# Optimization experiments

Hardware: AMD Instinct MI355X
Metric: run time of the kernel (lower is better)

Reference implementation:

```python
import jax, jax.numpy as jnp
import numpy as np

N = 100000      # nodes
E = 400000      # edges
DIN, DH, DOUT = 32, 128, 1
EPS = 1e-5


def _lin_init(key, fan_in, shape):
    s = 1.0 / np.sqrt(fan_in)
    return jax.random.uniform(key, shape, jnp.float32, -s, s)


def setup_inputs() -> dict:
    key = jax.random.key(0)
    ks = jax.random.split(key, 24)
    x = jax.random.normal(ks[0], (N, DIN), jnp.float32)
    edge_index = jax.random.randint(ks[1], (2, E), 0, N, dtype=jnp.int64)
    d = {"x": x, "edge_index": edge_index}
    dims = [(DIN, DH), (DH, DH), (DH, DOUT)]
    for i, (din, dout) in enumerate(dims, start=1):
        d[f"W{i}"] = _lin_init(ks[2 * i], din, (din, dout))
        d[f"b{i}"] = _lin_init(ks[2 * i + 1], din, (dout,))
        d[f"g{i}"] = jnp.ones((dout,), jnp.float32)    # BatchNorm weight
        d[f"bt{i}"] = jnp.zeros((dout,), jnp.float32)  # BatchNorm bias
        d[f"lw{i}"] = jnp.ones((dout,), jnp.float32)   # LayerNorm weight
        d[f"lb{i}"] = jnp.zeros((dout,), jnp.float32)  # LayerNorm bias
    return d


def reference(x, edge_index, W1, b1, g1, bt1, lw1, lb1,
              W2, b2, g2, bt2, lw2, lb2,
              W3, b3, g3, bt3, lw3, lb3):
    n = x.shape[0]
    loop = jnp.arange(n, dtype=edge_index.dtype)
    src = jnp.concatenate([edge_index[0], loop])  # self-loops added (GCNConv default)
    dst = jnp.concatenate([edge_index[1], loop])
    deg = jax.ops.segment_sum(jnp.ones(src.shape[0], x.dtype), dst, num_segments=n)
    dinv = jnp.where(deg > 0, jax.lax.rsqrt(deg), 0.0)
    norm = dinv[src] * dinv[dst]  # D^{-1/2} (A+I) D^{-1/2} edge weights

    def gcn(h, W, b):
        h = h @ W
        agg = jax.ops.segment_sum(h[src] * norm[:, None], dst, num_segments=n)
        return agg + b

    def bn(h, g, b):  # BatchNorm1d, training-mode batch stats (biased var)
        m = h.mean(0)
        v = h.var(0)
        return (h - m) * jax.lax.rsqrt(v + EPS) * g + b

    def inorm(h):  # PyG InstanceNorm, single graph, affine=False
        m = h.mean(0)
        v = h.var(0)
        return (h - m) * jax.lax.rsqrt(v + EPS)

    def lnorm(h, w, b):  # PyG LayerNorm, mode='graph': stats over all nodes+channels
        m = h.mean()
        v = h.var()
        return (h - m) * jax.lax.rsqrt(v + EPS) * w + b

    h = jax.nn.relu(lnorm(inorm(bn(gcn(x, W1, b1), g1, bt1)), lw1, lb1))
    h = jax.nn.relu(lnorm(inorm(bn(gcn(h, W2, b2), g2, bt2)), lw2, lb2))
    h = lnorm(inorm(bn(gcn(h, W3, b3), g3, bt3)), lw3, lb3)
    return h.flatten()
```

## Files before the change

kernel.cpp:

```cpp
#include <hip/hip_runtime.h>
#include <cstddef>

#define EPS 1e-5f

typedef __attribute__((ext_vector_type(8))) short bf16x8;
typedef __attribute__((ext_vector_type(8))) unsigned short u16x8;
typedef __attribute__((ext_vector_type(4))) float f32x4;

__device__ inline short f2bf(float f) {
    union { float f; unsigned u; } v;
    v.f = f;
    unsigned r = v.u + 0x7fff + ((v.u >> 16) & 1);
    return (short)(r >> 16);
}
__device__ inline float bf2f(unsigned short s) {
    union { unsigned u; float f; } v;
    v.u = ((unsigned)s) << 16;
    return v.f;
}

__global__ void prep_kernel(const float* __restrict__ W1, const float* __restrict__ W2,
                            unsigned short* __restrict__ Wt1, unsigned short* __restrict__ Wt2,
                            int* __restrict__ counts, float* __restrict__ sums,
                            unsigned long long* __restrict__ state, int* __restrict__ ticket,
                            int n) {
    int o = blockIdx.x * blockDim.x + threadIdx.x;
    if (o < n) counts[o] = 0;
    if (o < 516) sums[o] = 0.f;
    if (o < 128) state[o] = 0ULL;
    if (o == 0) *ticket = 0;
    if (o < 32 * 128) {
        int c = o / 32, k = o % 32;
        Wt1[o] = (unsigned short)f2bf(W1[(size_t)k * 128 + c]);
    } else if (o < 32 * 128 + 128 * 128) {
        int o2 = o - 32 * 128;
        int c = o2 / 128, k = o2 % 128;
        Wt2[o2] = (unsigned short)f2bf(W2[(size_t)k * 128 + c]);
    }
}

__global__ void hist_kernel(const int* __restrict__ dst, int E, int* __restrict__ counts) {
    int i = blockIdx.x * blockDim.x + threadIdx.x;
    if (i < E) atomicAdd(&counts[dst[i]], 1);
}

__global__ __launch_bounds__(1024) void scan_lookback(const int* __restrict__ counts,
                                                      int* __restrict__ rowptr,
                                                      int* __restrict__ cur,
                                                      float* __restrict__ dinv,
                                                      unsigned long long* __restrict__ state,
                                                      int* __restrict__ ticket, int n, int E) {
    __shared__ int sh[1024];
    __shared__ int sbid, sexcl;
    int t = threadIdx.x;
    if (t == 0) sbid = atomicAdd(ticket, 1);
    __syncthreads();
    int bid = sbid;
    int g = bid * 1024 + t;
    int v = (g < n) ? counts[g] : 0;
    sh[t] = v;
    __syncthreads();
    for (int off = 1; off < 1024; off <<= 1) {
        int add = (t >= off) ? sh[t - off] : 0;
        __syncthreads();
        sh[t] += add;
        __syncthreads();
    }
    int total = sh[1023];
    if (t == 0) {
        if (bid == 0) {
            atomicExch(&state[0], (2ULL << 32) | (unsigned)total);
            sexcl = 0;
        } else {
            atomicExch(&state[bid], (1ULL << 32) | (unsigned)total);
            int excl = 0;
            int j = bid - 1;
            while (true) {
                unsigned long long s;
                do { s = atomicAdd(&state[j], 0ULL); } while ((s >> 32) == 0);
                excl += (int)(s & 0xffffffffULL);
                if ((s >> 32) == 2ULL) break;
                j--;
            }
            atomicExch(&state[bid], (2ULL << 32) | (unsigned)(excl + total));
            sexcl = excl;
        }
    }
    __syncthreads();
    int excl = sexcl;
    if (g < n) {
        int r = excl + sh[t] - v;
        rowptr[g] = r;
        cur[g] = r;
        dinv[g] = rsqrtf((float)counts[g] + 1.0f);
    }
    if (g == 0) rowptr[n] = E;
}

__global__ void fill_kernel(const int* __restrict__ src, const int* __restrict__ dst, int E,
                            int* __restrict__ cur, const float* __restrict__ dinv,
                            int* __restrict__ esrc, float* __restrict__ ewt) {
    int e = blockIdx.x * blockDim.x + threadIdx.x;
    if (e < E) {
        int d = dst[e];
        int s = src[e];
        int p = atomicAdd(&cur[d], 1);
        esrc[p] = s;
        ewt[p] = dinv[s] * dinv[d];
    }
}

template <int K, bool NORM, bool STATS>
__global__ __launch_bounds__(256) void gemm_mfma(const unsigned short* __restrict__ hb,
                                                 const unsigned short* __restrict__ Wt,
                                                 const float* __restrict__ ss,
                                                 unsigned short* __restrict__ outb,
                                                 float* __restrict__ sums, int n) {
    int wid = (blockIdx.x * 256 + threadIdx.x) >> 6;
    int wv = (threadIdx.x >> 6);
    int lane = threadIdx.x & 63;
    int m = lane & 15;
    int qd = lane >> 4;
    int r0 = wid * 32;
    if (!STATS && r0 >= n) return;

    f32x4 acc[2][8];
#pragma unroll
    for (int rt = 0; rt < 2; rt++)
#pragma unroll
        for (int ct = 0; ct < 8; ct++) acc[rt][ct] = (f32x4){0.f, 0.f, 0.f, 0.f};

    if (r0 < n) {
#pragma unroll
        for (int q = 0; q < K / 32; q++) {
            int k0 = q * 32 + qd * 8;
            bf16x8 a[2];
#pragma unroll
            for (int rt = 0; rt < 2; rt++) {
                int r = r0 + rt * 16 + m;
                bf16x8 av = (bf16x8){0, 0, 0, 0, 0, 0, 0, 0};
                if (r < n) av = *(const bf16x8*)(hb + (size_t)r * K + k0);
                if (NORM) {
#pragma unroll
                    for (int j = 0; j < 8; j++) {
                        float f = bf2f((unsigned short)av[j]);
                        f = fmaxf(fmaf(f, ss[k0 + j], ss[K + k0 + j]), 0.f);
                        av[j] = f2bf(f);
                    }
                }
                a[rt] = av;
            }
#pragma unroll
            for (int ct = 0; ct < 8; ct++) {
                bf16x8 b = *(const bf16x8*)(Wt + (size_t)(ct * 16 + m) * K + k0);
                acc[0][ct] = __builtin_amdgcn_mfma_f32_16x16x32_bf16(a[0], b, acc[0][ct], 0, 0, 0);
                acc[1][ct] = __builtin_amdgcn_mfma_f32_16x16x32_bf16(a[1], b, acc[1][ct], 0, 0, 0);
            }
        }
#pragma unroll
        for (int rt = 0; rt < 2; rt++)
#pragma unroll
            for (int i = 0; i < 4; i++) {
                int r = r0 + rt * 16 + qd * 4 + i;
                if (r < n) {
#pragma unroll
                    for (int ct = 0; ct < 8; ct++)
                        outb[(size_t)r * 128 + ct * 16 + m] = (unsigned short)f2bf(acc[rt][ct][i]);
                }
            }
    }

    if (STATS) {
        __shared__ float ls[4][128], lq[4][128];
#pragma unroll
        for (int ct = 0; ct < 8; ct++) {
            float s = 0.f, q = 0.f;
#pragma unroll
            for (int rt = 0; rt < 2; rt++)
#pragma unroll
                for (int i = 0; i < 4; i++) {
                    float v = acc[rt][ct][i];
                    s += v;
                    q += v * v;
                }
            s += __shfl_xor(s, 16, 64);
            s += __shfl_xor(s, 32, 64);
            q += __shfl_xor(q, 16, 64);
            q += __shfl_xor(q, 32, 64);
            if (qd == 0) {
                ls[wv][ct * 16 + m] = s;
                lq[wv][ct * 16 + m] = q;
            }
        }
        __syncthreads();
        int t = threadIdx.x;
        if (t < 128) {
            atomicAdd(&sums[t], ls[0][t] + ls[1][t] + ls[2][t] + ls[3][t]);
        } else {
            int c = t - 128;
            atomicAdd(&sums[128 + c], lq[0][c] + lq[1][c] + lq[2][c] + lq[3][c]);
        }
    }
}

__global__ void gemv_norm_bf(const unsigned short* __restrict__ hb, const float* __restrict__ W,
                             const float* __restrict__ ss, float* __restrict__ out, int n) {
    int gid = blockIdx.x * blockDim.x + threadIdx.x;
    int wid = gid >> 6, lane = gid & 63;
    int nw = (gridDim.x * blockDim.x) >> 6;
    int c = lane * 2;
    float w0 = W[c], w1 = W[c + 1];
    float s0 = ss[c], s1 = ss[c + 1];
    float t0 = ss[128 + c], t1 = ss[128 + c + 1];
    for (int r = wid; r < n; r += nw) {
        ushort2 u = ((const ushort2*)(hb + (size_t)r * 128))[lane];
        float a = fmaxf(fmaf(bf2f(u.x), s0, t0), 0.f);
        float b = fmaxf(fmaf(bf2f(u.y), s1, t1), 0.f);
        float v = fmaf(a, w0, b * w1);
#pragma unroll
        for (int off = 32; off > 0; off >>= 1) v += __shfl_down(v, off, 64);
        if (lane == 0) out[r] = v;
    }
}

__global__ __launch_bounds__(256) void agg128_bf(const unsigned short* __restrict__ tmp,
                                                 const int* __restrict__ rowptr,
                                                 const int* __restrict__ esrc,
                                                 const float* __restrict__ ewt,
                                                 const float* __restrict__ dinv,
                                                 unsigned short* __restrict__ agg, int n) {
    int node = (blockIdx.x << 4) + (threadIdx.x >> 4);
    if (node >= n) return;
    int co = (threadIdx.x & 15) << 3;
    float di = dinv[node];
    float d2 = di * di;
    u16x8 t = *(const u16x8*)(tmp + ((size_t)node << 7) + co);
    float acc[8];
#pragma unroll
    for (int k = 0; k < 8; k++) acc[k] = bf2f(t[k]) * d2;
    int j = rowptr[node], je = rowptr[node + 1];
    for (; j + 8 <= je; j += 8) {
        int s[8];
        float w[8];
        u16x8 v[8];
#pragma unroll
        for (int k = 0; k < 8; k++) { s[k] = esrc[j + k]; w[k] = ewt[j + k]; }
#pragma unroll
        for (int k = 0; k < 8; k++) v[k] = *(const u16x8*)(tmp + ((size_t)s[k] << 7) + co);
#pragma unroll
        for (int k = 0; k < 8; k++)
#pragma unroll
            for (int c = 0; c < 8; c++) acc[c] = fmaf(bf2f(v[k][c]), w[k], acc[c]);
    }
    if (j + 4 <= je) {
        int s[4];
        float w[4];
        u16x8 v[4];
#pragma unroll
        for (int k = 0; k < 4; k++) { s[k] = esrc[j + k]; w[k] = ewt[j + k]; }
#pragma unroll
        for (int k = 0; k < 4; k++) v[k] = *(const u16x8*)(tmp + ((size_t)s[k] << 7) + co);
#pragma unroll
        for (int k = 0; k < 4; k++)
#pragma unroll
            for (int c = 0; c < 8; c++) acc[c] = fmaf(bf2f(v[k][c]), w[k], acc[c]);
        j += 4;
    }
    for (; j < je; j++) {
        int s = esrc[j];
        float w = ewt[j];
        u16x8 v = *(const u16x8*)(tmp + ((size_t)s << 7) + co);
#pragma unroll
        for (int c = 0; c < 8; c++) acc[c] = fmaf(bf2f(v[c]), w, acc[c]);
    }
    u16x8 o;
#pragma unroll
    for (int k = 0; k < 8; k++) o[k] = (unsigned short)f2bf(acc[k]);
    *(u16x8*)(agg + ((size_t)node << 7) + co) = o;
}

__global__ __launch_bounds__(256) void stats128_bf(const unsigned short* __restrict__ a,
                                                   float* __restrict__ sums, int n) {
    __shared__ float ls[16][128], lq[16][128];
    int t = threadIdx.x;
    int rg = t >> 4;
    int cg = t & 15;
    float s[8], q[8];
#pragma unroll
    for (int k = 0; k < 8; k++) { s[k] = 0.f; q[k] = 0.f; }
    for (int r = blockIdx.x * 16 + rg; r < n; r += gridDim.x * 16) {
        u16x8 v = *(const u16x8*)(a + (size_t)r * 128 + cg * 8);
#pragma unroll
        for (int k = 0; k < 8; k++) {
            float f = bf2f(v[k]);
            s[k] += f;
            q[k] = fmaf(f, f, q[k]);
        }
    }
#pragma unroll
    for (int k = 0; k < 8; k++) {
        ls[rg][cg * 8 + k] = s[k];
        lq[rg][cg * 8 + k] = q[k];
    }
    __syncthreads();
    if (t < 128) {
        float v = 0.f;
#pragma unroll
        for (int i = 0; i < 16; i++) v += ls[i][t];
        atomicAdd(&sums[t], v);
    } else {
        int c = t - 128;
        float v = 0.f;
#pragma unroll
        for (int i = 0; i < 16; i++) v += lq[i][c];
        atomicAdd(&sums[128 + c], v);
    }
}

__global__ __launch_bounds__(256) void agg32_f(const float* __restrict__ x,
                                               const int* __restrict__ rowptr,
                                               const int* __restrict__ esrc,
                                               const float* __restrict__ ewt,
                                               const float* __restrict__ dinv,
                                               unsigned short* __restrict__ xab, int n) {
    int g = threadIdx.x >> 3;
    int lane = threadIdx.x & 7;
    int node = blockIdx.x * 32 + g;
    if (node >= n) return;
    int co = lane << 2;
    float di = dinv[node];
    float d2 = di * di;
    float4 a = *(const float4*)(x + ((size_t)node << 5) + co);
    a.x *= d2; a.y *= d2; a.z *= d2; a.w *= d2;
    int j = rowptr[node], je = rowptr[node + 1];
    for (; j + 4 <= je; j += 4) {
        int s0 = esrc[j], s1 = esrc[j + 1], s2 = esrc[j + 2], s3 = esrc[j + 3];
        float w0 = ewt[j], w1 = ewt[j + 1], w2 = ewt[j + 2], w3 = ewt[j + 3];
        float4 v0 = *(const float4*)(x + ((size_t)s0 << 5) + co);
        float4 v1 = *(const float4*)(x + ((size_t)s1 << 5) + co);
        float4 v2 = *(const float4*)(x + ((size_t)s2 << 5) + co);
        float4 v3 = *(const float4*)(x + ((size_t)s3 << 5) + co);
        a.x = fmaf(v0.x, w0, a.x); a.y = fmaf(v0.y, w0, a.y);
        a.z = fmaf(v0.z, w0, a.z); a.w = fmaf(v0.w, w0, a.w);
        a.x = fmaf(v1.x, w1, a.x); a.y = fmaf(v1.y, w1, a.y);
        a.z = fmaf(v1.z, w1, a.z); a.w = fmaf(v1.w, w1, a.w);
        a.x = fmaf(v2.x, w2, a.x); a.y = fmaf(v2.y, w2, a.y);
        a.z = fmaf(v2.z, w2, a.z); a.w = fmaf(v2.w, w2, a.w);
        a.x = fmaf(v3.x, w3, a.x); a.y = fmaf(v3.y, w3, a.y);
        a.z = fmaf(v3.z, w3, a.z); a.w = fmaf(v3.w, w3, a.w);
    }
    for (; j < je; j++) {
        int s = esrc[j];
        float w = ewt[j];
        float4 v = *(const float4*)(x + ((size_t)s << 5) + co);
        a.x = fmaf(v.x, w, a.x); a.y = fmaf(v.y, w, a.y);
        a.z = fmaf(v.z, w, a.z); a.w = fmaf(v.w, w, a.w);
    }
    ushort4 o;
    o.x = (unsigned short)f2bf(a.x);
    o.y = (unsigned short)f2bf(a.y);
    o.z = (unsigned short)f2bf(a.z);
    o.w = (unsigned short)f2bf(a.w);
    ((ushort4*)(xab + ((size_t)node << 5)))[lane] = o;
}

__global__ void agg1_stats(const float* __restrict__ tmp, const int* __restrict__ rowptr,
                           const int* __restrict__ esrc, const float* __restrict__ ewt,
                           const float* __restrict__ dinv, float* __restrict__ out,
                           float* __restrict__ part, int n) {
    int i = blockIdx.x * blockDim.x + threadIdx.x;
    float acc = 0.f;
    if (i < n) {
        float di = dinv[i];
        acc = tmp[i] * di * di;
        int j = rowptr[i], je = rowptr[i + 1];
        for (; j + 4 <= je; j += 4) {
            int s0 = esrc[j], s1 = esrc[j + 1], s2 = esrc[j + 2], s3 = esrc[j + 3];
            float w0 = ewt[j], w1 = ewt[j + 1], w2 = ewt[j + 2], w3 = ewt[j + 3];
            float v0 = tmp[s0], v1 = tmp[s1], v2 = tmp[s2], v3 = tmp[s3];
            acc = fmaf(v0, w0, acc);
            acc = fmaf(v1, w1, acc);
            acc = fmaf(v2, w2, acc);
            acc = fmaf(v3, w3, acc);
        }
        for (; j < je; j++) acc = fmaf(tmp[esrc[j]], ewt[j], acc);
        out[i] = acc;
    }
    float s = acc, q = acc * acc;
#pragma unroll
    for (int off = 32; off > 0; off >>= 1) {
        s += __shfl_down(s, off, 64);
        q += __shfl_down(q, off, 64);
    }
    if ((threadIdx.x & 63) == 0) {
        int wgid = (blockIdx.x * blockDim.x + threadIdx.x) >> 6;
        part[2 * wgid] = s;
        part[2 * wgid + 1] = q;
    }
}

__global__ __launch_bounds__(256) void reduce_part(const float* __restrict__ part,
                                                   float* __restrict__ sums, int nw) {
    __shared__ float ls[256], lq[256];
    int t = threadIdx.x;
    float s = 0.f, q = 0.f;
    for (int i = t; i < nw; i += 256) {
        s += part[2 * i];
        q += part[2 * i + 1];
    }
    ls[t] = s;
    lq[t] = q;
    __syncthreads();
    for (int off = 128; off > 0; off >>= 1) {
        if (t < off) {
            ls[t] += ls[t + off];
            lq[t] += lq[t + off];
        }
        __syncthreads();
    }
    if (t == 0) {
        sums[0] = ls[0];
        sums[1] = lq[0];
    }
}

__global__ void apply1_kernel(const float* __restrict__ sums, const float* __restrict__ g,
                              const float* __restrict__ lw, const float* __restrict__ lb,
                              const float* __restrict__ a, float* __restrict__ out, int n) {
    int i = blockIdx.x * blockDim.x + threadIdx.x;
    if (i >= n) return;
    float m = sums[0] / n;
    float v = sums[1] / n - m * m;
    v = v < 0.f ? 0.f : v;
    float bs = rsqrtf(v + EPS) * g[0];
    float vz = v * bs * bs;
    float t = bs * rsqrtf(vz + EPS);
    float GV = v * t * t;
    float S = t * rsqrtf(GV + EPS) * lw[0];
    float T = lb[0] - m * S;
    out[i] = fmaf(a[i], S, T);
}

template <int C>
__global__ void finalize_kernel(const float* __restrict__ sums, const float* __restrict__ g,
                                const float* __restrict__ lw, const float* __restrict__ lb,
                                float* __restrict__ ss, int n) {
    __shared__ float vt2[C];
    int c = threadIdx.x;
    float m = sums[c] / n;
    float v = sums[C + c] / n - m * m;
    v = v < 0.f ? 0.f : v;
    float gc = g[c];
    float bs = rsqrtf(v + EPS) * gc;
    float vz = v * bs * bs;
    float t = bs * rsqrtf(vz + EPS);
    vt2[c] = v * t * t;
    __syncthreads();
    if (c == 0) {
        float gv = 0.f;
        for (int i = 0; i < C; i++) gv += vt2[i];
        vt2[0] = gv / C;
    }
    __syncthreads();
    float GV = vt2[0];
    float S = t * rsqrtf(GV + EPS) * lw[c];
    ss[c] = S;
    ss[C + c] = lb[c] - m * S;
}

extern "C" void kernel_launch(void* const* d_in, const int* in_sizes, int n_in,
                              void* d_out, int out_size, void* d_ws, size_t ws_size,
                              hipStream_t stream) {
    const float* x = (const float*)d_in[0];
    const int* ei = (const int*)d_in[1];
    int n = in_sizes[0] / 32;
    int E = in_sizes[1] / 2;
    const int* src = ei;
    const int* dstp = ei + E;
    const float* W1 = (const float*)d_in[2];
    const float* g1 = (const float*)d_in[4];
    const float* lw1 = (const float*)d_in[6];
    const float* lb1 = (const float*)d_in[7];
    const float* W2 = (const float*)d_in[8];
    const float* g2 = (const float*)d_in[10];
    const float* lw2 = (const float*)d_in[12];
    const float* lb2 = (const float*)d_in[13];
    const float* W3 = (const float*)d_in[14];
    const float* g3 = (const float*)d_in[16];
    const float* lw3 = (const float*)d_in[18];
    const float* lb3 = (const float*)d_in[19];
    float* out = (float*)d_out;

    char* p = (char*)d_ws;
    int* counts = (int*)p;             p += (size_t)n * 4;
    int* cur = (int*)p;                p += (size_t)n * 4;
    int* rowptr = (int*)p;             p += (size_t)(n + 4) * 4;
    unsigned long long* state = (unsigned long long*)p;  p += 128 * 8;
    int* ticket = (int*)p;             p += 4 * 4;
    int* esrc = (int*)p;               p += (size_t)E * 4;
    float* ewt = (float*)p;            p += (size_t)E * 4;
    float* dinv = (float*)p;           p += (size_t)n * 4;
    unsigned short* Wt1 = (unsigned short*)p;  p += 128 * 32 * 2;
    unsigned short* Wt2 = (unsigned short*)p;  p += 128 * 128 * 2;
    unsigned short* xa = (unsigned short*)p;   p += (size_t)n * 32 * 2;
    unsigned short* h1 = (unsigned short*)p;   p += (size_t)n * 128 * 2;
    unsigned short* t2 = (unsigned short*)p;   p += (size_t)n * 128 * 2;
    unsigned short* a2 = (unsigned short*)p;   p += (size_t)n * 128 * 2;
    float* t3 = (float*)p;             p += (size_t)n * 4;
    float* a3 = (float*)p;             p += (size_t)n * 4;
    float* sums1 = (float*)p;          p += 256 * 4;
    float* sums2 = (float*)p;          p += 256 * 4;
    float* sums3 = (float*)p;          p += 4 * 4;
    float* ss1 = (float*)p;            p += 256 * 4;
    float* ss2 = (float*)p;            p += 256 * 4;
    float* part3 = (float*)p;          p += ((size_t)(n + 255) / 256) * 4 * 2 * 4;

    int B = (n + 1023) / 1024;

    prep_kernel<<<(n + 255) / 256, 256, 0, stream>>>(W1, W2, Wt1, Wt2, counts, sums1,
                                                     state, ticket, n);
    hist_kernel<<<(E + 255) / 256, 256, 0, stream>>>(dstp, E, counts);
    scan_lookback<<<B, 1024, 0, stream>>>(counts, rowptr, cur, dinv, state, ticket, n, E);
    fill_kernel<<<(E + 255) / 256, 256, 0, stream>>>(src, dstp, E, cur, dinv, esrc, ewt);

    int mblk = ((n + 31) / 32 + 3) / 4;

    agg32_f<<<(n + 31) / 32, 256, 0, stream>>>(x, rowptr, esrc, ewt, dinv, xa, n);
    gemm_mfma<32, false, true><<<mblk, 256, 0, stream>>>(xa, Wt1, nullptr, h1, sums1, n);
    finalize_kernel<128><<<1, 128, 0, stream>>>(sums1, g1, lw1, lb1, ss1, n);

    gemm_mfma<128, true, false><<<mblk, 256, 0, stream>>>(h1, Wt2, ss1, t2, nullptr, n);
    agg128_bf<<<(n + 15) / 16, 256, 0, stream>>>(t2, rowptr, esrc, ewt, dinv, a2, n);
    stats128_bf<<<512, 256, 0, stream>>>(a2, sums2, n);
    finalize_kernel<128><<<1, 128, 0, stream>>>(sums2, g2, lw2, lb2, ss2, n);

    int ablk1 = (n + 255) / 256;
    gemv_norm_bf<<<1024, 256, 0, stream>>>(a2, W3, ss2, t3, n);
    agg1_stats<<<ablk1, 256, 0, stream>>>(t3, rowptr, esrc, ewt, dinv, a3, part3, n);
    reduce_part<<<1, 256, 0, stream>>>(part3, sums3, ablk1 * 4);
    apply1_kernel<<<(n + 255) / 256, 256, 0, stream>>>(sums3, g3, lw3, lb3, a3, out, n);
}
```

Before: 307.7 us.

## Pack edge src/weight into int2 and fuse norm finalize kernels into consumers

Edge source indices and normalized weights are stored together as int2 so the aggregation kernels issue one 8-byte load per edge instead of two separate loads. The standalone finalize and reduce kernels are removed: each consuming block (the second GEMM, the GEMV, and the final apply) recomputes the BN/InstanceNorm/LayerNorm scale/shift from the raw sums in shared memory. This drops several tiny launches and intermediate buffers, at the cost of redundant per-block finalize work and an extra serial reduction plus barriers at block start.

```diff
diff --git a/kernel.cpp b/kernel.cpp
--- a/kernel.cpp
+++ b/kernel.cpp
@@ -26,7 +26,7 @@
                             int n) {
     int o = blockIdx.x * blockDim.x + threadIdx.x;
     if (o < n) counts[o] = 0;
-    if (o < 516) sums[o] = 0.f;
+    if (o < 512) sums[o] = 0.f;
     if (o < 128) state[o] = 0ULL;
     if (o == 0) *ticket = 0;
     if (o < 32 * 128) {
@@ -99,23 +99,60 @@
 
 __global__ void fill_kernel(const int* __restrict__ src, const int* __restrict__ dst, int E,
                             int* __restrict__ cur, const float* __restrict__ dinv,
-                            int* __restrict__ esrc, float* __restrict__ ewt) {
+                            int2* __restrict__ edge) {
     int e = blockIdx.x * blockDim.x + threadIdx.x;
     if (e < E) {
         int d = dst[e];
         int s = src[e];
         int p = atomicAdd(&cur[d], 1);
-        esrc[p] = s;
-        ewt[p] = dinv[s] * dinv[d];
-    }
+        edge[p] = make_int2(s, __float_as_int(dinv[s] * dinv[d]));
+    }
+}
+
+__device__ inline void finalize_ch(float sum, float sumsq, float g, int n,
+                                   float& m, float& t, float& vt2) {
+    m = sum / n;
+    float v = sumsq / n - m * m;
+    v = v < 0.f ? 0.f : v;
+    float bs = rsqrtf(v + EPS) * g;
+    float vz = v * bs * bs;
+    t = bs * rsqrtf(vz + EPS);
+    vt2 = v * t * t;
 }
 
 template <int K, bool NORM, bool STATS>
 __global__ __launch_bounds__(256) void gemm_mfma(const unsigned short* __restrict__ hb,
                                                  const unsigned short* __restrict__ Wt,
-                                                 const float* __restrict__ ss,
+                                                 const float* __restrict__ sums_in,
+                                                 const float* __restrict__ gw,
+                                                 const float* __restrict__ lw,
+                                                 const float* __restrict__ lb,
                                                  unsigned short* __restrict__ outb,
-                                                 float* __restrict__ sums, int n) {
+                                                 float* __restrict__ sums_out, int n) {
+    __shared__ float sh_ss[NORM ? 256 : 1];
+    __shared__ float sh_v[NORM ? 128 : 1];
+    if (NORM) {
+        int t = threadIdx.x;
+        float m, tt, vt2;
+        if (t < 128) {
+            finalize_ch(sums_in[t], sums_in[128 + t], gw[t], n, m, tt, vt2);
+            sh_v[t] = vt2;
+        }
+        __syncthreads();
+        if (t == 0) {
+            float gv = 0.f;
+            for (int i = 0; i < 128; i++) gv += sh_v[i];
+            sh_v[0] = gv / 128.f;
+        }
+        __syncthreads();
+        if (t < 128) {
+            float S = tt * rsqrtf(sh_v[0] + EPS) * lw[t];
+            sh_ss[t] = S;
+            sh_ss[128 + t] = lb[t] - m * S;
+        }
+        __syncthreads();
+    }
+
     int wid = (blockIdx.x * 256 + threadIdx.x) >> 6;
     int wv = (threadIdx.x >> 6);
     int lane = threadIdx.x & 63;
@@ -144,7 +181,7 @@
 #pragma unroll
                     for (int j = 0; j < 8; j++) {
                         float f = bf2f((unsigned short)av[j]);
-                        f = fmaxf(fmaf(f, ss[k0 + j], ss[K + k0 + j]), 0.f);
+                        f = fmaxf(fmaf(f, sh_ss[k0 + j], sh_ss[K + k0 + j]), 0.f);
                         av[j] = f2bf(f);
                     }
                 }
@@ -195,23 +232,51 @@
         __syncthreads();
         int t = threadIdx.x;
         if (t < 128) {
-            atomicAdd(&sums[t], ls[0][t] + ls[1][t] + ls[2][t] + ls[3][t]);
+            atomicAdd(&sums_out[t], ls[0][t] + ls[1][t] + ls[2][t] + ls[3][t]);
         } else {
             int c = t - 128;
-            atomicAdd(&sums[128 + c], lq[0][c] + lq[1][c] + lq[2][c] + lq[3][c]);
-        }
-    }
-}
-
-__global__ void gemv_norm_bf(const unsigned short* __restrict__ hb, const float* __restrict__ W,
-                             const float* __restrict__ ss, float* __restrict__ out, int n) {
+            atomicAdd(&sums_out[128 + c], lq[0][c] + lq[1][c] + lq[2][c] + lq[3][c]);
+        }
+    }
+}
+
+__global__ __launch_bounds__(256) void gemv_norm_bf(const unsigned short* __restrict__ hb,
+                                                    const float* __restrict__ W,
+                                                    const float* __restrict__ sums_in,
+                                                    const float* __restrict__ gw,
+                                                    const float* __restrict__ lw,
+                                                    const float* __restrict__ lb,
+                                                    float* __restrict__ out, int n) {
+    __shared__ float sh_ss[256];
+    __shared__ float sh_v[128];
+    {
+        int t = threadIdx.x;
+        float m, tt, vt2;
+        if (t < 128) {
+            finalize_ch(sums_in[t], sums_in[128 + t], gw[t], n, m, tt, vt2);
+            sh_v[t] = vt2;
+        }
+        __syncthreads();
+        if (t == 0) {
+            float gv = 0.f;
+            for (int i = 0; i < 128; i++) gv += sh_v[i];
+            sh_v[0] = gv / 128.f;
+        }
+        __syncthreads();
+        if (t < 128) {
+            float S = tt * rsqrtf(sh_v[0] + EPS) * lw[t];
+            sh_ss[t] = S;
+            sh_ss[128 + t] = lb[t] - m * S;
+        }
+        __syncthreads();
+    }
     int gid = blockIdx.x * blockDim.x + threadIdx.x;
     int wid = gid >> 6, lane = gid & 63;
     int nw = (gridDim.x * blockDim.x) >> 6;
     int c = lane * 2;
     float w0 = W[c], w1 = W[c + 1];
-    float s0 = ss[c], s1 = ss[c + 1];
-    float t0 = ss[128 + c], t1 = ss[128 + c + 1];
+    float s0 = sh_ss[c], s1 = sh_ss[c + 1];
+    float t0 = sh_ss[128 + c], t1 = sh_ss[128 + c + 1];
     for (int r = wid; r < n; r += nw) {
         ushort2 u = ((const ushort2*)(hb + (size_t)r * 128))[lane];
         float a = fmaxf(fmaf(bf2f(u.x), s0, t0), 0.f);
@@ -225,8 +290,7 @@
 
 __global__ __launch_bounds__(256) void agg128_bf(const unsigned short* __restrict__ tmp,
                                                  const int* __restrict__ rowptr,
-                                                 const int* __restrict__ esrc,
-                                                 const float* __restrict__ ewt,
+                                                 const int2* __restrict__ edge,
                                                  const float* __restrict__ dinv,
                                                  unsigned short* __restrict__ agg, int n) {
     int node = (blockIdx.x << 4) + (threadIdx.x >> 4);
@@ -240,36 +304,38 @@
     for (int k = 0; k < 8; k++) acc[k] = bf2f(t[k]) * d2;
     int j = rowptr[node], je = rowptr[node + 1];
     for (; j + 8 <= je; j += 8) {
-        int s[8];
-        float w[8];
+        int2 e[8];
         u16x8 v[8];
 #pragma unroll
-        for (int k = 0; k < 8; k++) { s[k] = esrc[j + k]; w[k] = ewt[j + k]; }
-#pragma unroll
-        for (int k = 0; k < 8; k++) v[k] = *(const u16x8*)(tmp + ((size_t)s[k] << 7) + co);
-#pragma unroll
-        for (int k = 0; k < 8; k++)
-#pragma unroll
-            for (int c = 0; c < 8; c++) acc[c] = fmaf(bf2f(v[k][c]), w[k], acc[c]);
+        for (int k = 0; k < 8; k++) e[k] = edge[j + k];
+#pragma unroll
+        for (int k = 0; k < 8; k++) v[k] = *(const u16x8*)(tmp + ((size_t)e[k].x << 7) + co);
+#pragma unroll
+        for (int k = 0; k < 8; k++) {
+            float w = __int_as_float(e[k].y);
+#pragma unroll
+            for (int c = 0; c < 8; c++) acc[c] = fmaf(bf2f(v[k][c]), w, acc[c]);
+        }
     }
     if (j + 4 <= je) {
-        int s[4];
-        float w[4];
+        int2 e[4];
         u16x8 v[4];
 #pragma unroll
-        for (int k = 0; k < 4; k++) { s[k] = esrc[j + k]; w[k] = ewt[j + k]; }
-#pragma unroll
-        for (int k = 0; k < 4; k++) v[k] = *(const u16x8*)(tmp + ((size_t)s[k] << 7) + co);
-#pragma unroll
-        for (int k = 0; k < 4; k++)
-#pragma unroll
-            for (int c = 0; c < 8; c++) acc[c] = fmaf(bf2f(v[k][c]), w[k], acc[c]);
+        for (int k = 0; k < 4; k++) e[k] = edge[j + k];
+#pragma unroll
+        for (int k = 0; k < 4; k++) v[k] = *(const u16x8*)(tmp + ((size_t)e[k].x << 7) + co);
+#pragma unroll
+        for (int k = 0; k < 4; k++) {
+            float w = __int_as_float(e[k].y);
+#pragma unroll
+            for (int c = 0; c < 8; c++) acc[c] = fmaf(bf2f(v[k][c]), w, acc[c]);
+        }
         j += 4;
     }
     for (; j < je; j++) {
-        int s = esrc[j];
-        float w = ewt[j];
-        u16x8 v = *(const u16x8*)(tmp + ((size_t)s << 7) + co);
+        int2 e = edge[j];
+        float w = __int_as_float(e.y);
+        u16x8 v = *(const u16x8*)(tmp + ((size_t)e.x << 7) + co);
 #pragma unroll
         for (int c = 0; c < 8; c++) acc[c] = fmaf(bf2f(v[c]), w, acc[c]);
     }
@@ -319,8 +385,7 @@
 
 __global__ __launch_bounds__(256) void agg32_f(const float* __restrict__ x,
                                                const int* __restrict__ rowptr,
-                                               const int* __restrict__ esrc,
-                                               const float* __restrict__ ewt,
+                                               const int2* __restrict__ edge,
                                                const float* __restrict__ dinv,
                                                unsigned short* __restrict__ xab, int n) {
     int g = threadIdx.x >> 3;
@@ -334,12 +399,13 @@
     a.x *= d2; a.y *= d2; a.z *= d2; a.w *= d2;
     int j = rowptr[node], je = rowptr[node + 1];
     for (; j + 4 <= je; j += 4) {
-        int s0 = esrc[j], s1 = esrc[j + 1], s2 = esrc[j + 2], s3 = esrc[j + 3];
-        float w0 = ewt[j], w1 = ewt[j + 1], w2 = ewt[j + 2], w3 = ewt[j + 3];
-        float4 v0 = *(const float4*)(x + ((size_t)s0 << 5) + co);
-        float4 v1 = *(const float4*)(x + ((size_t)s1 << 5) + co);
-        float4 v2 = *(const float4*)(x + ((size_t)s2 << 5) + co);
-        float4 v3 = *(const float4*)(x + ((size_t)s3 << 5) + co);
+        int2 e0 = edge[j], e1 = edge[j + 1], e2 = edge[j + 2], e3 = edge[j + 3];
+        float4 v0 = *(const float4*)(x + ((size_t)e0.x << 5) + co);
+        float4 v1 = *(const float4*)(x + ((size_t)e1.x << 5) + co);
+        float4 v2 = *(const float4*)(x + ((size_t)e2.x << 5) + co);
+        float4 v3 = *(const float4*)(x + ((size_t)e3.x << 5) + co);
+        float w0 = __int_as_float(e0.y), w1 = __int_as_float(e1.y);
+        float w2 = __int_as_float(e2.y), w3 = __int_as_float(e3.y);
         a.x = fmaf(v0.x, w0, a.x); a.y = fmaf(v0.y, w0, a.y);
         a.z = fmaf(v0.z, w0, a.z); a.w = fmaf(v0.w, w0, a.w);
         a.x = fmaf(v1.x, w1, a.x); a.y = fmaf(v1.y, w1, a.y);
@@ -350,9 +416,9 @@
         a.z = fmaf(v3.z, w3, a.z); a.w = fmaf(v3.w, w3, a.w);
     }
     for (; j < je; j++) {
-        int s = esrc[j];
-        float w = ewt[j];
-        float4 v = *(const float4*)(x + ((size_t)s << 5) + co);
+        int2 e = edge[j];
+        float w = __int_as_float(e.y);
+        float4 v = *(const float4*)(x + ((size_t)e.x << 5) + co);
         a.x = fmaf(v.x, w, a.x); a.y = fmaf(v.y, w, a.y);
         a.z = fmaf(v.z, w, a.z); a.w = fmaf(v.w, w, a.w);
     }
@@ -365,9 +431,8 @@
 }
 
 __global__ void agg1_stats(const float* __restrict__ tmp, const int* __restrict__ rowptr,
-                           const int* __restrict__ esrc, const float* __restrict__ ewt,
-                           const float* __restrict__ dinv, float* __restrict__ out,
-                           float* __restrict__ part, int n) {
+                           const int2* __restrict__ edge, const float* __restrict__ dinv,
+                           float* __restrict__ out, float* __restrict__ part, int n) {
     int i = blockIdx.x * blockDim.x + threadIdx.x;
     float acc = 0.f;
     if (i < n) {
@@ -375,15 +440,17 @@
         acc = tmp[i] * di * di;
         int j = rowptr[i], je = rowptr[i + 1];
         for (; j + 4 <= je; j += 4) {
-            int s0 = esrc[j], s1 = esrc[j + 1], s2 = esrc[j + 2], s3 = esrc[j + 3];
-            float w0 = ewt[j], w1 = ewt[j + 1], w2 = ewt[j + 2], w3 = ewt[j + 3];
-            float v0 = tmp[s0], v1 = tmp[s1], v2 = tmp[s2], v3 = tmp[s3];
-            acc = fmaf(v0, w0, acc);
-            acc = fmaf(v1, w1, acc);
-            acc = fmaf(v2, w2, acc);
-            acc = fmaf(v3, w3, acc);
-        }
-        for (; j < je; j++) acc = fmaf(tmp[esrc[j]], ewt[j], acc);
+            int2 e0 = edge[j], e1 = edge[j + 1], e2 = edge[j + 2], e3 = edge[j + 3];
+            float v0 = tmp[e0.x], v1 = tmp[e1.x], v2 = tmp[e2.x], v3 = tmp[e3.x];
+            acc = fmaf(v0, __int_as_float(e0.y), acc);
+            acc = fmaf(v1, __int_as_float(e1.y), acc);
+            acc = fmaf(v2, __int_as_float(e2.y), acc);
+            acc = fmaf(v3, __int_as_float(e3.y), acc);
+        }
+        for (; j < je; j++) {
+            int2 e = edge[j];
+            acc = fmaf(tmp[e.x], __int_as_float(e.y), acc);
+        }
         out[i] = acc;
     }
     float s = acc, q = acc * acc;
@@ -399,8 +466,12 @@
     }
 }
 
-__global__ __launch_bounds__(256) void reduce_part(const float* __restrict__ part,
-                                                   float* __restrict__ sums, int nw) {
+__global__ __launch_bounds__(256) void apply1_kernel(const float* __restrict__ part, int nw,
+                                                     const float* __restrict__ g,
+                                                     const float* __restrict__ lw,
+                                                     const float* __restrict__ lb,
+                                                     const float* __restrict__ a,
+                                                     float* __restrict__ out, int n) {
     __shared__ float ls[256], lq[256];
     int t = threadIdx.x;
     float s = 0.f, q = 0.f;
@@ -418,54 +489,17 @@
         }
         __syncthreads();
     }
-    if (t == 0) {
-        sums[0] = ls[0];
-        sums[1] = lq[0];
-    }
-}
-
-__global__ void apply1_kernel(const float* __restrict__ sums, const float* __restrict__ g,
-                              const float* __restrict__ lw, const float* __restrict__ lb,
-                              const float* __restrict__ a, float* __restrict__ out, int n) {
-    int i = blockIdx.x * blockDim.x + threadIdx.x;
-    if (i >= n) return;
-    float m = sums[0] / n;
-    float v = sums[1] / n - m * m;
+    float m = ls[0] / n;
+    float v = lq[0] / n - m * m;
     v = v < 0.f ? 0.f : v;
     float bs = rsqrtf(v + EPS) * g[0];
     float vz = v * bs * bs;
-    float t = bs * rsqrtf(vz + EPS);
-    float GV = v * t * t;
-    float S = t * rsqrtf(GV + EPS) * lw[0];
+    float tt = bs * rsqrtf(vz + EPS);
+    float GV = v * tt * tt;
+    float S = tt * rsqrtf(GV + EPS) * lw[0];
     float T = lb[0] - m * S;
-    out[i] = fmaf(a[i], S, T);
-}
-
-template <int C>
-__global__ void finalize_kernel(const float* __restrict__ sums, const float* __restrict__ g,
-                                const float* __restrict__ lw, const float* __restrict__ lb,
-                                float* __restrict__ ss, int n) {
-    __shared__ float vt2[C];
-    int c = threadIdx.x;
-    float m = sums[c] / n;
-    float v = sums[C + c] / n - m * m;
-    v = v < 0.f ? 0.f : v;
-    float gc = g[c];
-    float bs = rsqrtf(v + EPS) * gc;
-    float vz = v * bs * bs;
-    float t = bs * rsqrtf(vz + EPS);
-    vt2[c] = v * t * t;
-    __syncthreads();
-    if (c == 0) {
-        float gv = 0.f;
-        for (int i = 0; i < C; i++) gv += vt2[i];
-        vt2[0] = gv / C;
-    }
-    __syncthreads();
-    float GV = vt2[0];
-    float S = t * rsqrtf(GV + EPS) * lw[c];
-    ss[c] = S;
-    ss[C + c] = lb[c] - m * S;
+    int i = blockIdx.x * blockDim.x + t;
+    if (i < n) out[i] = fmaf(a[i], S, T);
 }
 
 extern "C" void kernel_launch(void* const* d_in, const int* in_sizes, int n_in,
@@ -497,8 +531,7 @@
     int* rowptr = (int*)p;             p += (size_t)(n + 4) * 4;
     unsigned long long* state = (unsigned long long*)p;  p += 128 * 8;
     int* ticket = (int*)p;             p += 4 * 4;
-    int* esrc = (int*)p;               p += (size_t)E * 4;
-    float* ewt = (float*)p;            p += (size_t)E * 4;
+    int2* edge = (int2*)p;             p += (size_t)E * 8;
     float* dinv = (float*)p;           p += (size_t)n * 4;
     unsigned short* Wt1 = (unsigned short*)p;  p += 128 * 32 * 2;
     unsigned short* Wt2 = (unsigned short*)p;  p += 128 * 128 * 2;
@@ -510,9 +543,6 @@
     float* a3 = (float*)p;             p += (size_t)n * 4;
     float* sums1 = (float*)p;          p += 256 * 4;
     float* sums2 = (float*)p;          p += 256 * 4;
-    float* sums3 = (float*)p;          p += 4 * 4;
-    float* ss1 = (float*)p;            p += 256 * 4;
-    float* ss2 = (float*)p;            p += 256 * 4;
     float* part3 = (float*)p;          p += ((size_t)(n + 255) / 256) * 4 * 2 * 4;
 
     int B = (n + 1023) / 1024;
@@ -521,22 +551,21 @@
                                                      state, ticket, n);
     hist_kernel<<<(E + 255) / 256, 256, 0, stream>>>(dstp, E, counts);
     scan_lookback<<<B, 1024, 0, stream>>>(counts, rowptr, cur, dinv, state, ticket, n, E);
-    fill_kernel<<<(E + 255) / 256, 256, 0, stream>>>(src, dstp, E, cur, dinv, esrc, ewt);
+    fill_kernel<<<(E + 255) / 256, 256, 0, stream>>>(src, dstp, E, cur, dinv, edge);
 
     int mblk = ((n + 31) / 32 + 3) / 4;
 
-    agg32_f<<<(n + 31) / 32, 256, 0, stream>>>(x, rowptr, esrc, ewt, dinv, xa, n);
-    gemm_mfma<32, false, true><<<mblk, 256, 0, stream>>>(xa, Wt1, nullptr, h1, sums1, n);
-    finalize_kernel<128><<<1, 128, 0, stream>>>(sums1, g1, lw1, lb1, ss1, n);
-
-    gemm_mfma<128, true, false><<<mblk, 256, 0, stream>>>(h1, Wt2, ss1, t2, nullptr, n);
-    agg128_bf<<<(n + 15) / 16, 256, 0, stream>>>(t2, rowptr, esrc, ewt, dinv, a2, n);
+    agg32_f<<<(n + 31) / 32, 256, 0, stream>>>(x, rowptr, edge, dinv, xa, n);
+    gemm_mfma<32, false, true><<<mblk, 256, 0, stream>>>(xa, Wt1, nullptr, nullptr, nullptr,
+                                                         nullptr, h1, sums1, n);
+
+    gemm_mfma<128, true, false><<<mblk, 256, 0, stream>>>(h1, Wt2, sums1, g1, lw1, lb1,
+                                                          t2, nullptr, n);
+    agg128_bf<<<(n + 15) / 16, 256, 0, stream>>>(t2, rowptr, edge, dinv, a2, n);
     stats128_bf<<<512, 256, 0, stream>>>(a2, sums2, n);
-    finalize_kernel<128><<<1, 128, 0, stream>>>(sums2, g2, lw2, lb2, ss2, n);
 
     int ablk1 = (n + 255) / 256;
-    gemv_norm_bf<<<1024, 256, 0, stream>>>(a2, W3, ss2, t3, n);
-    agg1_stats<<<ablk1, 256, 0, stream>>>(t3, rowptr, esrc, ewt, dinv, a3, part3, n);
-    reduce_part<<<1, 256, 0, stream>>>(part3, sums3, ablk1 * 4);
-    apply1_kernel<<<(n + 255) / 256, 256, 0, stream>>>(sums3, g3, lw3, lb3, a3, out, n);
-}
+    gemv_norm_bf<<<1024, 256, 0, stream>>>(a2, W3, sums2, g2, lw2, lb2, t3, n);
+    agg1_stats<<<ablk1, 256, 0, stream>>>(t3, rowptr, edge, dinv, a3, part3, n);
+    apply1_kernel<<<ablk1, 256, 0, stream>>>(part3, ablk1 * 4, g3, lw3, lb3, a3, out, n);
+}
```

Measured after the change: 300.8 us. 1.02x faster.
